# Kernel optimization log

Hardware: AMD Instinct MI355X
Metric: run time of the kernel (lower is better)

## Reference

```python
import jax, jax.numpy as jnp
import numpy as np

NEG_SLOPE = 0.2  # PyG GATv2Conv default negative_slope
N_NODES = 50000
N_EDGES = 600000
N_GRAPHS = 512


def gatv2_layer(x, src, dst, Wl, bl, Wr, br, att, bias, n_nodes, heads, out_ch):
    """PyG GATv2Conv (concat=False -> mean over heads). src/dst include self-loops."""
    xl = (x @ Wl + bl).reshape(n_nodes, heads, out_ch)  # source transform
    xr = (x @ Wr + br).reshape(n_nodes, heads, out_ch)  # target transform
    e = jax.nn.leaky_relu(xl[src] + xr[dst], NEG_SLOPE)          # [E, H, C]
    logits = jnp.einsum('ehc,hc->eh', e, att)                     # [E, H]
    # segment softmax over destination node
    amax = jax.ops.segment_max(logits, dst, num_segments=n_nodes)  # [N, H]
    amax = jnp.where(jnp.isfinite(amax), amax, 0.0)
    ex = jnp.exp(logits - amax[dst])
    denom = jax.ops.segment_sum(ex, dst, num_segments=n_nodes)
    alpha = ex / jnp.clip(denom[dst], 1e-16)                      # [E, H]
    msg = xl[src] * alpha[:, :, None]                             # [E, H, C]
    out = jax.ops.segment_sum(msg, dst, num_segments=n_nodes)     # [N, H, C]
    return out.mean(axis=1) + bias                                # [N, C]


def setup_inputs() -> dict:
    key = jax.random.key(0)
    ks = jax.random.split(key, 20)
    s = 0.1
    x = jax.random.normal(ks[0], (N_NODES, 7), dtype=jnp.float32)
    edge_index = jax.random.randint(ks[1], (2, N_EDGES), 0, N_NODES, dtype=jnp.int64)
    batch = jnp.sort(jax.random.randint(ks[2], (N_NODES,), 0, N_GRAPHS, dtype=jnp.int64))
    H1, C1 = 2, 64   # conv1: 7 -> 64, heads=2
    H2, C2 = 2, 64   # conv2: 64 -> 64, heads=2
    H3, C3 = 1, 128  # conv3: 64 -> 128, heads=1
    p = {
        'W1l': jax.random.normal(ks[3], (7, H1 * C1)) * s,
        'b1l': jnp.zeros((H1 * C1,), jnp.float32),
        'W1r': jax.random.normal(ks[4], (7, H1 * C1)) * s,
        'b1r': jnp.zeros((H1 * C1,), jnp.float32),
        'att1': jax.random.normal(ks[5], (H1, C1)) * s,
        'bias1': jnp.zeros((C1,), jnp.float32),
        'W2l': jax.random.normal(ks[6], (C1, H2 * C2)) * s,
        'b2l': jnp.zeros((H2 * C2,), jnp.float32),
        'W2r': jax.random.normal(ks[7], (C1, H2 * C2)) * s,
        'b2r': jnp.zeros((H2 * C2,), jnp.float32),
        'att2': jax.random.normal(ks[8], (H2, C2)) * s,
        'bias2': jnp.zeros((C2,), jnp.float32),
        'W3l': jax.random.normal(ks[9], (C2, H3 * C3)) * s,
        'b3l': jnp.zeros((H3 * C3,), jnp.float32),
        'W3r': jax.random.normal(ks[10], (C2, H3 * C3)) * s,
        'b3r': jnp.zeros((H3 * C3,), jnp.float32),
        'att3': jax.random.normal(ks[11], (H3, C3)) * s,
        'bias3': jnp.zeros((C3,), jnp.float32),
        'Wc': jax.random.normal(ks[12], (C3, 11)) * s,
        'bc': jnp.zeros((11,), jnp.float32),
    }
    return {'x': x, 'edge_index': edge_index, 'batch': batch, **p}


def reference(x, edge_index, batch,
              W1l, b1l, W1r, b1r, att1, bias1,
              W2l, b2l, W2r, b2r, att2, bias2,
              W3l, b3l, W3r, b3r, att3, bias3,
              Wc, bc):
    n = x.shape[0]
    # GATv2Conv default add_self_loops=True (same augmented edge set each layer)
    loop = jnp.arange(n, dtype=edge_index.dtype)
    src = jnp.concatenate([edge_index[0], loop])
    dst = jnp.concatenate([edge_index[1], loop])

    h = jax.nn.elu(gatv2_layer(x, src, dst, W1l, b1l, W1r, b1r, att1, bias1, n, 2, 64))
    h = jax.nn.elu(gatv2_layer(h, src, dst, W2l, b2l, W2r, b2r, att2, bias2, n, 2, 64))
    h = gatv2_layer(h, src, dst, W3l, b3l, W3r, b3r, att3, bias3, n, 1, 128)

    # global mean pool over graphs
    sums = jax.ops.segment_sum(h, batch, num_segments=N_GRAPHS)          # [G, 128]
    cnt = jax.ops.segment_sum(jnp.ones((n,), h.dtype), batch, num_segments=N_GRAPHS)
    graph_embed = sums / jnp.clip(cnt, 1.0)[:, None]
    return graph_embed @ Wc + bc                                         # [G, 11]
```

## Files before the change

### kernel.cpp

```cpp
#include <hip/hip_runtime.h>
#include <hip/hip_bf16.h>
#include <math.h>


#define PAD_SHIFT 6


__global__ void build_csr(const int* __restrict__ edge_src, const int* __restrict__ edge_dst,
                          int* __restrict__ cnt, int* __restrict__ csr, int NE, int E) {
    int e = blockIdx.x * blockDim.x + threadIdx.x;
    if (e >= E) return;
    int s, d;
    if (e < NE) { s = edge_src[e]; d = edge_dst[e]; }
    else        { s = d = e - NE; }
    int pos = atomicAdd(&cnt[d], 1) & 63;
    csr[(d << PAD_SHIFT) + pos] = s;
}


template<int IN_CH, int NPW>
__global__ __launch_bounds__(256) void transform_tile(
        const float* __restrict__ in,
        const float* __restrict__ Wl, const float* __restrict__ bl,
        const float* __restrict__ Wr, const float* __restrict__ br,
        ushort* __restrict__ xlh, float* __restrict__ xr, int n) {
    constexpr int NPB = 4 * NPW;
    __shared__ alignas(16) float rows[NPB][IN_CH];
    int tid = threadIdx.x;
    int t = tid & 63, w = tid >> 6;
    int n0 = blockIdx.x * NPB;

    if constexpr (IN_CH % 4 == 0) {
        constexpr int K4 = IN_CH / 4;
        for (int idx = tid; idx < NPB * K4; idx += 256) {
            int nn = idx / K4, k4 = idx - nn * K4;
            int node = n0 + nn; if (node > n - 1) node = n - 1;
            ((float4*)rows[nn])[k4] = ((const float4*)(in + (size_t)node * IN_CH))[k4];
        }
    } else {
        for (int idx = tid; idx < NPB * IN_CH; idx += 256) {
            int nn = idx / IN_CH, k = idx - nn * IN_CH;
            int node = n0 + nn; if (node > n - 1) node = n - 1;
            rows[nn][k] = in[(size_t)node * IN_CH + k];
        }
    }
    __syncthreads();

    int nb = w * NPW;
    float accl0[NPW], accl1[NPW], accr0[NPW], accr1[NPW];
    float bl0 = bl[t], bl1 = bl[t + 64], br0 = br[t], br1 = br[t + 64];
#pragma unroll
    for (int nn = 0; nn < NPW; ++nn) {
        accl0[nn] = bl0; accl1[nn] = bl1; accr0[nn] = br0; accr1[nn] = br1;
    }

    if constexpr (IN_CH % 4 == 0) {
        constexpr int K4 = IN_CH / 4;
        for (int k4 = 0; k4 < K4; ++k4) {
            float wl0[4], wl1[4], wr0[4], wr1[4];
#pragma unroll
            for (int j = 0; j < 4; ++j) {
                wl0[j] = Wl[(k4 * 4 + j) * 128 + t];
                wl1[j] = Wl[(k4 * 4 + j) * 128 + t + 64];
                wr0[j] = Wr[(k4 * 4 + j) * 128 + t];
                wr1[j] = Wr[(k4 * 4 + j) * 128 + t + 64];
            }
#pragma unroll
            for (int nn = 0; nn < NPW; ++nn) {
                float4 r = ((const float4*)rows[nb + nn])[k4];
                accl0[nn] = fmaf(r.x, wl0[0], accl0[nn]);
                accl1[nn] = fmaf(r.x, wl1[0], accl1[nn]);
                accr0[nn] = fmaf(r.x, wr0[0], accr0[nn]);
                accr1[nn] = fmaf(r.x, wr1[0], accr1[nn]);
                accl0[nn] = fmaf(r.y, wl0[1], accl0[nn]);
                accl1[nn] = fmaf(r.y, wl1[1], accl1[nn]);
                accr0[nn] = fmaf(r.y, wr0[1], accr0[nn]);
                accr1[nn] = fmaf(r.y, wr1[1], accr1[nn]);
                accl0[nn] = fmaf(r.z, wl0[2], accl0[nn]);
                accl1[nn] = fmaf(r.z, wl1[2], accl1[nn]);
                accr0[nn] = fmaf(r.z, wr0[2], accr0[nn]);
                accr1[nn] = fmaf(r.z, wr1[2], accr1[nn]);
                accl0[nn] = fmaf(r.w, wl0[3], accl0[nn]);
                accl1[nn] = fmaf(r.w, wl1[3], accl1[nn]);
                accr0[nn] = fmaf(r.w, wr0[3], accr0[nn]);
                accr1[nn] = fmaf(r.w, wr1[3], accr1[nn]);
            }
        }
    } else {
#pragma unroll
        for (int k = 0; k < IN_CH; ++k) {
            float wl0 = Wl[k * 128 + t], wl1 = Wl[k * 128 + t + 64];
            float wr0 = Wr[k * 128 + t], wr1 = Wr[k * 128 + t + 64];
#pragma unroll
            for (int nn = 0; nn < NPW; ++nn) {
                float xv = rows[nb + nn][k];
                accl0[nn] = fmaf(xv, wl0, accl0[nn]);
                accl1[nn] = fmaf(xv, wl1, accl1[nn]);
                accr0[nn] = fmaf(xv, wr0, accr0[nn]);
                accr1[nn] = fmaf(xv, wr1, accr1[nn]);
            }
        }
    }

#pragma unroll
    for (int nn = 0; nn < NPW; ++nn) {
        int node = n0 + nb + nn;
        if (node < n) {
            __hip_bfloat16* hl = (__hip_bfloat16*)(xlh + ((size_t)node << 7));
            float* orr = xr + ((size_t)node << 7);
            hl[t]      = __float2bfloat16(accl0[nn]);
            hl[t + 64] = __float2bfloat16(accl1[nn]);
            orr[t] = accr0[nn]; orr[t + 64] = accr1[nn];
        }
    }
}


template<int CTRL>
__device__ __forceinline__ float dpp_add(float v) {
    int x = __builtin_amdgcn_update_dpp(0, __float_as_int(v), CTRL, 0xF, 0xF, true);
    return v + __int_as_float(x);
}
__device__ __forceinline__ float reduce8(float v) {
    v = dpp_add<0xB1>(v);
    v = dpp_add<0x4E>(v);
    v = dpp_add<0x141>(v);
    return v;
}
__device__ __forceinline__ float reduce16(float v) {
    v = reduce8(v);
    v = dpp_add<0x140>(v);
    return v;
}


__device__ __forceinline__ void unpack8(const uint4& u, float c[8]) {
    c[0] = __int_as_float((int)(u.x << 16));
    c[1] = __int_as_float((int)(u.x & 0xffff0000u));
    c[2] = __int_as_float((int)(u.y << 16));
    c[3] = __int_as_float((int)(u.y & 0xffff0000u));
    c[4] = __int_as_float((int)(u.z << 16));
    c[5] = __int_as_float((int)(u.z & 0xffff0000u));
    c[6] = __int_as_float((int)(u.w << 16));
    c[7] = __int_as_float((int)(u.w & 0xffff0000u));
}


#define AGG_PH(CUR, FRE)                                                       \
    {                                                                          \
        int tf0 = srcof(it + 2 * EPI + g);                                     \
        int tf1 = srcof(it + 2 * EPI + 4 + g);                                 \
        FRE[0] = *(const uint4*)(xlh + ((size_t)tf0 << 7) + (q << 3));         \
        FRE[1] = *(const uint4*)(xlh + ((size_t)tf1 << 7) + (q << 3));         \
        _Pragma("unroll")                                                      \
        for (int j = 0; j < 2; ++j) {                                          \
            float c[8]; unpack8(CUR[j], c);                                    \
            float p = 0.f;                                                     \
            _Pragma("unroll")                                                  \
            for (int k = 0; k < 8; ++k) {                                      \
                float tt = c[k] + xrv[k];                                      \
                p = fmaf(tt > 0.f ? atv[k] : atw[k], tt, p);                   \
            }                                                                  \
            p = TWOHEAD ? reduce8(p) : reduce16(p);                            \
            float w = (it + j * 4 + g) < deg ? exp2f(p) : 0.f;                 \
            ssum += w;                                                         \
            _Pragma("unroll")                                                  \
            for (int k = 0; k < 8; ++k) acc[k] = fmaf(w, c[k], acc[k]);        \
        }                                                                      \
        it += EPI;                                                             \
    }

template<bool TWOHEAD>
__global__ void gat_agg_fused(const ushort* __restrict__ xlh, const float* __restrict__ xr,
                              const float* __restrict__ att, const float* __restrict__ bias,
                              const int* __restrict__ cnt, const int* __restrict__ csr,
                              float* __restrict__ outbuf, int n) {
    constexpr int EPI = 8;
    constexpr float L2E = 1.4426950408889634f;
    int wid = (blockIdx.x * blockDim.x + threadIdx.x) >> 6;
    if (wid >= n) return;
    int node = wid;
    int lane = threadIdx.x & 63;
    int g = lane >> 4, q = lane & 15;

    float xrv[8], atv[8], atw[8], acc[8];
    {
        const float4* xp = (const float4*)(xr + ((size_t)node << 7) + q * 8);
        const float4* ap = (const float4*)(att + q * 8);
        float4 x0 = xp[0], x1 = xp[1], a0 = ap[0], a1 = ap[1];
        xrv[0]=x0.x; xrv[1]=x0.y; xrv[2]=x0.z; xrv[3]=x0.w;
        xrv[4]=x1.x; xrv[5]=x1.y; xrv[6]=x1.z; xrv[7]=x1.w;
        atv[0]=a0.x*L2E; atv[1]=a0.y*L2E; atv[2]=a0.z*L2E; atv[3]=a0.w*L2E;
        atv[4]=a1.x*L2E; atv[5]=a1.y*L2E; atv[6]=a1.z*L2E; atv[7]=a1.w*L2E;
#pragma unroll
        for (int k = 0; k < 8; ++k) { atw[k] = 0.2f * atv[k]; acc[k] = 0.f; }
    }

    int deg = cnt[node]; if (deg > 64) deg = 64;
    int idxvec = csr[((size_t)node << PAD_SHIFT) + lane];
    auto srcof = [&](int p) { return __shfl(idxvec, p < deg ? p : 0, 64); };

    uint4 X[2], Y[2], Z[2];
    {
        int s00 = srcof(g), s01 = srcof(4 + g);
        int s10 = srcof(EPI + g), s11 = srcof(EPI + 4 + g);
        X[0] = *(const uint4*)(xlh + ((size_t)s00 << 7) + (q << 3));
        X[1] = *(const uint4*)(xlh + ((size_t)s01 << 7) + (q << 3));
        Y[0] = *(const uint4*)(xlh + ((size_t)s10 << 7) + (q << 3));
        Y[1] = *(const uint4*)(xlh + ((size_t)s11 << 7) + (q << 3));
    }

    float ssum = 0.f;
    int it = 0;
    while (true) {
        AGG_PH(X, Z)
        if (it >= deg) break;
        AGG_PH(Y, X)
        if (it >= deg) break;
        AGG_PH(Z, Y)
        if (it >= deg) break;
    }

    ssum += __shfl_xor(ssum, 32, 64);
    ssum += __shfl_xor(ssum, 16, 64);
#pragma unroll
    for (int k = 0; k < 8; ++k) {
        acc[k] += __shfl_xor(acc[k], 32, 64);
        acc[k] += __shfl_xor(acc[k], 16, 64);
    }

    float inv = 1.f / ssum;
    if constexpr (TWOHEAD) {
        float o[8];
#pragma unroll
        for (int k = 0; k < 8; ++k) {
            float r = acc[k] * inv;
            float ro = __shfl_xor(r, 8, 64);
            float v = 0.5f * (r + ro) + bias[(q & 7) * 8 + k];
            o[k] = (v > 0.f) ? v : expm1f(v);
        }
        if (lane < 8) {
            float4* op = (float4*)(outbuf + (size_t)node * 64 + q * 8);
            op[0] = make_float4(o[0], o[1], o[2], o[3]);
            op[1] = make_float4(o[4], o[5], o[6], o[7]);
        }
    } else {
        float o[8];
#pragma unroll
        for (int k = 0; k < 8; ++k) o[k] = acc[k] * inv + bias[q * 8 + k];
        if (lane < 16) {
            float4* op = (float4*)(outbuf + ((size_t)node << 7) + q * 8);
            op[0] = make_float4(o[0], o[1], o[2], o[3]);
            op[1] = make_float4(o[4], o[5], o[6], o[7]);
        }
    }
}


__device__ __forceinline__ int lower_bound(const int* __restrict__ a, int n, int key) {
    int lo = 0, hi = n;
    while (lo < hi) {
        int mid = (lo + hi) >> 1;
        if (a[mid] < key) lo = mid + 1; else hi = mid;
    }
    return lo;
}

__global__ void pool_kernel(const float* __restrict__ h3, const int* __restrict__ batch,
                            const float* __restrict__ Wc, const float* __restrict__ bc,
                            float* __restrict__ out, int n, int G) {
    int g = blockIdx.x;
    int tid = threadIdx.x;
    __shared__ float mean[128];
    int start = lower_bound(batch, n, g);
    int end   = lower_bound(batch, n, g + 1);
    float s0 = 0.f, s1 = 0.f, s2 = 0.f, s3 = 0.f;
    int node = start;
    for (; node + 3 < end; node += 4) {
        s0 += h3[(size_t)node * 128 + tid];
        s1 += h3[(size_t)(node + 1) * 128 + tid];
        s2 += h3[(size_t)(node + 2) * 128 + tid];
        s3 += h3[(size_t)(node + 3) * 128 + tid];
    }
    for (; node < end; ++node) s0 += h3[(size_t)node * 128 + tid];
    float s = (s0 + s1) + (s2 + s3);
    int cnt = end - start;
    float mv = s / (float)(cnt > 0 ? cnt : 1);
    mean[tid] = mv;
    __syncthreads();
    if (tid < 11) {
        float o = bc[tid];
        for (int c = 0; c < 128; ++c) o += mean[c] * Wc[c * 11 + tid];
        out[g * 11 + tid] = o;
    }
}


extern "C" void kernel_launch(void* const* d_in, const int* in_sizes, int n_in,
                              void* d_out, int out_size, void* d_ws, size_t ws_size,
                              hipStream_t stream) {
    const float* x     = (const float*)d_in[0];
    const int*   ei    = (const int*)d_in[1];
    const int*   batch = (const int*)d_in[2];
    const float* W1l = (const float*)d_in[3],  *b1l = (const float*)d_in[4];
    const float* W1r = (const float*)d_in[5],  *b1r = (const float*)d_in[6];
    const float* att1 = (const float*)d_in[7], *bias1 = (const float*)d_in[8];
    const float* W2l = (const float*)d_in[9],  *b2l = (const float*)d_in[10];
    const float* W2r = (const float*)d_in[11], *b2r = (const float*)d_in[12];
    const float* att2 = (const float*)d_in[13], *bias2 = (const float*)d_in[14];
    const float* W3l = (const float*)d_in[15], *b3l = (const float*)d_in[16];
    const float* W3r = (const float*)d_in[17], *b3r = (const float*)d_in[18];
    const float* att3 = (const float*)d_in[19], *bias3 = (const float*)d_in[20];
    const float* Wc  = (const float*)d_in[21], *bc  = (const float*)d_in[22];
    float* out = (float*)d_out;

    const int N  = in_sizes[0] / 7;
    const int NE = in_sizes[1] / 2;
    const int E  = NE + N;
    const int G  = out_size / 11;

    const int* edge_src = ei;
    const int* edge_dst = ei + NE;

    char* p = (char*)d_ws;
    auto alloc = [&](size_t bytes) { void* r = (void*)p; p += (bytes + 255) & ~(size_t)255; return r; };
    int*    cnt  = (int*)alloc((size_t)N * sizeof(int));
    int*    csr  = (int*)alloc((size_t)N * 64 * sizeof(int));
    ushort* xlh  = (ushort*)alloc((size_t)N * 128 * sizeof(ushort));
    float*  xr   = (float*)alloc((size_t)N * 128 * sizeof(float));
    float*  hbuf = (float*)alloc((size_t)N * 128 * sizeof(float));

    (void)hipMemsetAsync(cnt, 0, (size_t)N * sizeof(int), stream);
    build_csr<<<(E + 255) / 256, 256, 0, stream>>>(edge_src, edge_dst, cnt, csr, NE, E);

    const int NPB = 32;
    int tgrid = (N + NPB - 1) / NPB;
    int agrid = (N + 3) / 4;

    transform_tile<7, 8><<<tgrid, 256, 0, stream>>>(x, W1l, b1l, W1r, b1r, xlh, xr, N);
    gat_agg_fused<true><<<agrid, 256, 0, stream>>>(xlh, xr, att1, bias1, cnt, csr, hbuf, N);

    transform_tile<64, 8><<<tgrid, 256, 0, stream>>>(hbuf, W2l, b2l, W2r, b2r, xlh, xr, N);
    gat_agg_fused<true><<<agrid, 256, 0, stream>>>(xlh, xr, att2, bias2, cnt, csr, hbuf, N);

    transform_tile<64, 8><<<tgrid, 256, 0, stream>>>(hbuf, W3l, b3l, W3r, b3r, xlh, xr, N);
    gat_agg_fused<false><<<agrid, 256, 0, stream>>>(xlh, xr, att3, bias3, cnt, csr, hbuf, N);

    pool_kernel<<<G, 128, 0, stream>>>(hbuf, batch, Wc, bc, out, N, G);
}
```

Baseline: 283.5 us.

## Remap aggregation lanes to 4-channel bf16 chunks with per-head lane groups

Changes the lane-to-data mapping in the fused GATv2 aggregation kernel. Each lane now loads 8-byte (4-channel) bf16 chunks instead of 16-byte ones, and in the two-head case lanes are split by head, so every logit reduction uses a uniform 16-lane DPP reduce. The aim is a more even load layout and a single reduction pattern, with fewer edges handled per iteration in the two-head case. The trade-off is more, smaller gather instructions, which could hurt memory efficiency.

```diff
diff --git a/kernel.cpp b/kernel.cpp
--- a/kernel.cpp
+++ b/kernel.cpp
@@ -121,52 +121,64 @@
     int x = __builtin_amdgcn_update_dpp(0, __float_as_int(v), CTRL, 0xF, 0xF, true);
     return v + __int_as_float(x);
 }
-__device__ __forceinline__ float reduce8(float v) {
+__device__ __forceinline__ float reduce16(float v) {
     v = dpp_add<0xB1>(v);
     v = dpp_add<0x4E>(v);
     v = dpp_add<0x141>(v);
-    return v;
-}
-__device__ __forceinline__ float reduce16(float v) {
-    v = reduce8(v);
     v = dpp_add<0x140>(v);
     return v;
 }
 
 
-__device__ __forceinline__ void unpack8(const uint4& u, float c[8]) {
+__device__ __forceinline__ void unpack4(const uint2& u, float c[4]) {
     c[0] = __int_as_float((int)(u.x << 16));
     c[1] = __int_as_float((int)(u.x & 0xffff0000u));
     c[2] = __int_as_float((int)(u.y << 16));
     c[3] = __int_as_float((int)(u.y & 0xffff0000u));
-    c[4] = __int_as_float((int)(u.z << 16));
-    c[5] = __int_as_float((int)(u.z & 0xffff0000u));
-    c[6] = __int_as_float((int)(u.w << 16));
-    c[7] = __int_as_float((int)(u.w & 0xffff0000u));
-}
-
-
-#define AGG_PH(CUR, FRE)                                                       \
+}
+
+
+__device__ __forceinline__ float chan4v(float p, const float c[4], const float xv[4],
+                                        const float a[4], const float a2[4]) {
+#pragma unroll
+    for (int k = 0; k < 4; ++k) {
+        float t = c[k] + xv[k];
+        p = fmaf(t > 0.f ? a[k] : a2[k], t, p);
+    }
+    return p;
+}
+__device__ __forceinline__ void acc4v(float acc[4], float w, const float c[4]) {
+#pragma unroll
+    for (int k = 0; k < 4; ++k) acc[k] = fmaf(w, c[k], acc[k]);
+}
+
+
+#define AGG_PH(CUR0, CUR1, FRE0, FRE1)                                         \
     {                                                                          \
-        int tf0 = srcof(it + 2 * EPI + g);                                     \
-        int tf1 = srcof(it + 2 * EPI + 4 + g);                                 \
-        FRE[0] = *(const uint4*)(xlh + ((size_t)tf0 << 7) + (q << 3));         \
-        FRE[1] = *(const uint4*)(xlh + ((size_t)tf1 << 7) + (q << 3));         \
-        _Pragma("unroll")                                                      \
-        for (int j = 0; j < 2; ++j) {                                          \
-            float c[8]; unpack8(CUR[j], c);                                    \
-            float p = 0.f;                                                     \
-            _Pragma("unroll")                                                  \
-            for (int k = 0; k < 8; ++k) {                                      \
-                float tt = c[k] + xrv[k];                                      \
-                p = fmaf(tt > 0.f ? atv[k] : atw[k], tt, p);                   \
-            }                                                                  \
-            p = TWOHEAD ? reduce8(p) : reduce16(p);                            \
-            float w = (it + j * 4 + g) < deg ? exp2f(p) : 0.f;                 \
-            ssum += w;                                                         \
-            _Pragma("unroll")                                                  \
-            for (int k = 0; k < 8; ++k) acc[k] = fmaf(w, c[k], acc[k]);        \
+        int tf0 = srcof(it + 2 * EPI + eg);                                    \
+        int tf1 = srcof(it + 2 * EPI + STEP + eg);                             \
+        FRE0[0] = *(const uint2*)(xlh + ((size_t)tf0 << 7) + rowo);            \
+        FRE0[1] = *(const uint2*)(xlh + ((size_t)tf1 << 7) + rowo);            \
+        if constexpr (!TWOHEAD) {                                              \
+            FRE1[0] = *(const uint2*)(xlh + ((size_t)tf0 << 7) + rowo + 64);   \
+            FRE1[1] = *(const uint2*)(xlh + ((size_t)tf1 << 7) + rowo + 64);   \
         }                                                                      \
+        bool v0 = (it + eg) < deg, v1 = (it + STEP + eg) < deg;                \
+        float ca[4], cb[4], da[4], db[4];                                      \
+        unpack4(CUR0[0], ca); unpack4(CUR0[1], cb);                            \
+        float pa = chan4v(0.f, ca, xrv0, atv0, atw0);                          \
+        float pb = chan4v(0.f, cb, xrv0, atv0, atw0);                          \
+        if constexpr (!TWOHEAD) {                                              \
+            unpack4(CUR1[0], da); unpack4(CUR1[1], db);                        \
+            pa = chan4v(pa, da, xrv1, atv1, atw1);                             \
+            pb = chan4v(pb, db, xrv1, atv1, atw1);                             \
+        }                                                                      \
+        pa = reduce16(pa); pb = reduce16(pb);                                  \
+        float w0 = v0 ? exp2f(pa) : 0.f;                                       \
+        float w1 = v1 ? exp2f(pb) : 0.f;                                       \
+        ssum += w0 + w1;                                                       \
+        acc4v(acc0, w0, ca); acc4v(acc0, w1, cb);                              \
+        if constexpr (!TWOHEAD) { acc4v(acc1, w0, da); acc4v(acc1, w1, db); }  \
         it += EPI;                                                             \
     }
 
@@ -175,83 +187,104 @@
                               const float* __restrict__ att, const float* __restrict__ bias,
                               const int* __restrict__ cnt, const int* __restrict__ csr,
                               float* __restrict__ outbuf, int n) {
-    constexpr int EPI = 8;
+    constexpr int STEP = TWOHEAD ? 2 : 4;
+    constexpr int EPI  = 2 * STEP;
     constexpr float L2E = 1.4426950408889634f;
     int wid = (blockIdx.x * blockDim.x + threadIdx.x) >> 6;
     if (wid >= n) return;
     int node = wid;
     int lane = threadIdx.x & 63;
     int g = lane >> 4, q = lane & 15;
-
-    float xrv[8], atv[8], atw[8], acc[8];
+    int eg   = TWOHEAD ? (g >> 1) : g;
+    int head = TWOHEAD ? (g & 1)  : 0;
+    int rowo = TWOHEAD ? (head * 64 + q * 4) : (q * 4);
+
+    float xrv0[4], atv0[4], atw0[4], acc0[4];
+    float xrv1[4], atv1[4], atw1[4], acc1[4];
     {
-        const float4* xp = (const float4*)(xr + ((size_t)node << 7) + q * 8);
-        const float4* ap = (const float4*)(att + q * 8);
-        float4 x0 = xp[0], x1 = xp[1], a0 = ap[0], a1 = ap[1];
-        xrv[0]=x0.x; xrv[1]=x0.y; xrv[2]=x0.z; xrv[3]=x0.w;
-        xrv[4]=x1.x; xrv[5]=x1.y; xrv[6]=x1.z; xrv[7]=x1.w;
-        atv[0]=a0.x*L2E; atv[1]=a0.y*L2E; atv[2]=a0.z*L2E; atv[3]=a0.w*L2E;
-        atv[4]=a1.x*L2E; atv[5]=a1.y*L2E; atv[6]=a1.z*L2E; atv[7]=a1.w*L2E;
-#pragma unroll
-        for (int k = 0; k < 8; ++k) { atw[k] = 0.2f * atv[k]; acc[k] = 0.f; }
+        float4 x0 = *(const float4*)(xr + ((size_t)node << 7) + rowo);
+        float4 a0 = *(const float4*)(att + rowo);
+        xrv0[0]=x0.x; xrv0[1]=x0.y; xrv0[2]=x0.z; xrv0[3]=x0.w;
+        atv0[0]=a0.x*L2E; atv0[1]=a0.y*L2E; atv0[2]=a0.z*L2E; atv0[3]=a0.w*L2E;
+#pragma unroll
+        for (int k = 0; k < 4; ++k) { atw0[k] = 0.2f * atv0[k]; acc0[k] = 0.f; }
+        if constexpr (!TWOHEAD) {
+            float4 x1 = *(const float4*)(xr + ((size_t)node << 7) + rowo + 64);
+            float4 a1 = *(const float4*)(att + rowo + 64);
+            xrv1[0]=x1.x; xrv1[1]=x1.y; xrv1[2]=x1.z; xrv1[3]=x1.w;
+            atv1[0]=a1.x*L2E; atv1[1]=a1.y*L2E; atv1[2]=a1.z*L2E; atv1[3]=a1.w*L2E;
+#pragma unroll
+            for (int k = 0; k < 4; ++k) { atw1[k] = 0.2f * atv1[k]; acc1[k] = 0.f; }
+        }
     }
 
     int deg = cnt[node]; if (deg > 64) deg = 64;
     int idxvec = csr[((size_t)node << PAD_SHIFT) + lane];
     auto srcof = [&](int p) { return __shfl(idxvec, p < deg ? p : 0, 64); };
 
-    uint4 X[2], Y[2], Z[2];
+    uint2 X0[2], X1[2], Y0[2], Y1[2], Z0[2], Z1[2];
     {
-        int s00 = srcof(g), s01 = srcof(4 + g);
-        int s10 = srcof(EPI + g), s11 = srcof(EPI + 4 + g);
-        X[0] = *(const uint4*)(xlh + ((size_t)s00 << 7) + (q << 3));
-        X[1] = *(const uint4*)(xlh + ((size_t)s01 << 7) + (q << 3));
-        Y[0] = *(const uint4*)(xlh + ((size_t)s10 << 7) + (q << 3));
-        Y[1] = *(const uint4*)(xlh + ((size_t)s11 << 7) + (q << 3));
+        int s00 = srcof(eg), s01 = srcof(STEP + eg);
+        int s10 = srcof(EPI + eg), s11 = srcof(EPI + STEP + eg);
+        X0[0] = *(const uint2*)(xlh + ((size_t)s00 << 7) + rowo);
+        X0[1] = *(const uint2*)(xlh + ((size_t)s01 << 7) + rowo);
+        Y0[0] = *(const uint2*)(xlh + ((size_t)s10 << 7) + rowo);
+        Y0[1] = *(const uint2*)(xlh + ((size_t)s11 << 7) + rowo);
+        if constexpr (!TWOHEAD) {
+            X1[0] = *(const uint2*)(xlh + ((size_t)s00 << 7) + rowo + 64);
+            X1[1] = *(const uint2*)(xlh + ((size_t)s01 << 7) + rowo + 64);
+            Y1[0] = *(const uint2*)(xlh + ((size_t)s10 << 7) + rowo + 64);
+            Y1[1] = *(const uint2*)(xlh + ((size_t)s11 << 7) + rowo + 64);
+        }
     }
 
     float ssum = 0.f;
     int it = 0;
     while (true) {
-        AGG_PH(X, Z)
+        AGG_PH(X0, X1, Z0, Z1)
         if (it >= deg) break;
-        AGG_PH(Y, X)
+        AGG_PH(Y0, Y1, X0, X1)
         if (it >= deg) break;
-        AGG_PH(Z, Y)
+        AGG_PH(Z0, Z1, Y0, Y1)
         if (it >= deg) break;
     }
 
     ssum += __shfl_xor(ssum, 32, 64);
-    ssum += __shfl_xor(ssum, 16, 64);
-#pragma unroll
-    for (int k = 0; k < 8; ++k) {
-        acc[k] += __shfl_xor(acc[k], 32, 64);
-        acc[k] += __shfl_xor(acc[k], 16, 64);
+#pragma unroll
+    for (int k = 0; k < 4; ++k) acc0[k] += __shfl_xor(acc0[k], 32, 64);
+    if constexpr (!TWOHEAD) {
+        ssum += __shfl_xor(ssum, 16, 64);
+#pragma unroll
+        for (int k = 0; k < 4; ++k) {
+            acc1[k] += __shfl_xor(acc1[k], 32, 64);
+            acc0[k] += __shfl_xor(acc0[k], 16, 64);
+            acc1[k] += __shfl_xor(acc1[k], 16, 64);
+        }
     }
 
     float inv = 1.f / ssum;
     if constexpr (TWOHEAD) {
-        float o[8];
-#pragma unroll
-        for (int k = 0; k < 8; ++k) {
-            float r = acc[k] * inv;
-            float ro = __shfl_xor(r, 8, 64);
-            float v = 0.5f * (r + ro) + bias[(q & 7) * 8 + k];
+        float o[4];
+#pragma unroll
+        for (int k = 0; k < 4; ++k) {
+            float r = acc0[k] * inv;
+            float ro = __shfl_xor(r, 16, 64);
+            float v = 0.5f * (r + ro) + bias[q * 4 + k];
             o[k] = (v > 0.f) ? v : expm1f(v);
         }
-        if (lane < 8) {
-            float4* op = (float4*)(outbuf + (size_t)node * 64 + q * 8);
-            op[0] = make_float4(o[0], o[1], o[2], o[3]);
-            op[1] = make_float4(o[4], o[5], o[6], o[7]);
-        }
+        if (lane < 16)
+            ((float4*)(outbuf + (size_t)node * 64))[q] = make_float4(o[0], o[1], o[2], o[3]);
     } else {
-        float o[8];
-#pragma unroll
-        for (int k = 0; k < 8; ++k) o[k] = acc[k] * inv + bias[q * 8 + k];
+        float o0[4], o1[4];
+#pragma unroll
+        for (int k = 0; k < 4; ++k) {
+            o0[k] = acc0[k] * inv + bias[q * 4 + k];
+            o1[k] = acc1[k] * inv + bias[q * 4 + 64 + k];
+        }
         if (lane < 16) {
-            float4* op = (float4*)(outbuf + ((size_t)node << 7) + q * 8);
-            op[0] = make_float4(o[0], o[1], o[2], o[3]);
-            op[1] = make_float4(o[4], o[5], o[6], o[7]);
+            float4* op = (float4*)(outbuf + ((size_t)node << 7));
+            op[q]      = make_float4(o0[0], o0[1], o0[2], o0[3]);
+            op[q + 16] = make_float4(o1[0], o1[1], o1[2], o1[3]);
         }
     }
 }
```

Result: faster. 248.4 us (-12.4%).
